# Kernel tuning notes

Hardware: AMD Instinct MI355X
Metric: run time of the kernel (lower is better)

## Reference

```python
import jax, jax.numpy as jnp
import numpy as np

MAX_DISP = 10
KS = 2 * MAX_DISP + 1  # 21 -> 441 displacements


def setup_inputs() -> dict:
    key = jax.random.key(0)
    k1, k2 = jax.random.split(key)
    B, C, H, W = 4, 64, 128, 128
    feat1 = jax.random.normal(k1, (B, C, H, W), dtype=jnp.float32)
    feat2 = jax.random.normal(k2, (B, C, H, W), dtype=jnp.float32)
    return {"feat1": feat1, "feat2": feat2}


def _correlation(feat1, feat2):
    B, C, H, W = feat1.shape
    pad = MAX_DISP
    feat2_p = jnp.pad(feat2, ((0, 0), (0, 0), (pad, pad), (pad, pad)))

    # all (i, j) displacements, flattened row-major to match torch cat order
    ii, jj = jnp.meshgrid(jnp.arange(KS), jnp.arange(KS), indexing="ij")
    shifts = jnp.stack([ii.ravel(), jj.ravel()], axis=-1)  # [KS*KS, 2]

    def one_shift(ij):
        i, j = ij[0], ij[1]
        f2 = jax.lax.dynamic_slice(feat2_p, (0, 0, i, j), (B, C, H, W))
        # reduce over channel dim only; avoid materializing product per-shift
        return jnp.einsum("bchw,bchw->bhw", feat1, f2) / C

    corr = jax.vmap(one_shift)(shifts)            # [KS*KS, B, H, W]
    return jnp.transpose(corr, (1, 0, 2, 3))      # [B, KS*KS, H, W]


def reference(feat1, feat2):
    return _correlation(feat1, feat2)
```

## Files before the change

### kernel.cpp

```cpp
#include <hip/hip_runtime.h>

#define BB  4
#define CC  64
#define HH  128
#define WW  128
#define KS  21
#define PAD 10

__global__ __launch_bounds__(256) void corr_kernel(
    const float* __restrict__ feat1,
    const float* __restrict__ feat2,
    float* __restrict__ out)
{
    const int tid = threadIdx.x;
    int bi = blockIdx.x;
    const int di = bi % KS;  bi /= KS;
    const int h8 = bi % (HH / 8);
    const int b  = bi / (HH / 8);

    const int h  = h8 * 8 + (tid >> 5);
    const int w0 = (tid & 31) << 2;

    const int r = h + di - PAD;

    float acc[4][KS];
#pragma unroll
    for (int p = 0; p < 4; ++p)
#pragma unroll
        for (int d = 0; d < KS; ++d) acc[p][d] = 0.0f;

    if (r >= 0 && r < HH) {
        const float* f1p = feat1 + ((size_t)(b * CC) * HH + h) * WW + w0;
        const float* f2p = feat2 + ((size_t)(b * CC) * HH + r) * WW;

#pragma unroll 2
        for (int c = 0; c < CC; ++c) {
            const float4 a = *(const float4*)(f1p + (size_t)c * (HH * WW));

            float win[28];
#pragma unroll
            for (int j = 0; j < 7; ++j) {
                const int off = w0 - 12 + 4 * j;
                float4 v = make_float4(0.f, 0.f, 0.f, 0.f);
                if (off >= 0 && off < WW)
                    v = *(const float4*)(f2p + (size_t)c * (HH * WW) + off);
                win[4 * j + 0] = v.x;
                win[4 * j + 1] = v.y;
                win[4 * j + 2] = v.z;
                win[4 * j + 3] = v.w;
            }

#pragma unroll
            for (int d = 0; d < KS; ++d) {
                acc[0][d] += a.x * win[d + 2];
                acc[1][d] += a.y * win[d + 3];
                acc[2][d] += a.z * win[d + 4];
                acc[3][d] += a.w * win[d + 5];
            }
        }
    }

    const float scale = 1.0f / (float)CC;
    float* op = out + (((size_t)b * (KS * KS) + (size_t)di * KS) * HH + h) * WW + w0;
#pragma unroll
    for (int d = 0; d < KS; ++d) {
        float4 v = make_float4(acc[0][d] * scale, acc[1][d] * scale,
                               acc[2][d] * scale, acc[3][d] * scale);
        *(float4*)(op + (size_t)d * (HH * WW)) = v;
    }
}

extern "C" void kernel_launch(void* const* d_in, const int* in_sizes, int n_in,
                              void* d_out, int out_size, void* d_ws, size_t ws_size,
                              hipStream_t stream) {
    const float* feat1 = (const float*)d_in[0];
    const float* feat2 = (const float*)d_in[1];
    float* out = (float*)d_out;

    const int blocks = BB * (HH / 8) * KS;
    corr_kernel<<<blocks, 256, 0, stream>>>(feat1, feat2, out);
}
```

Measured before the change: 228.9 us.

## Share feat2 row window through LDS and software-prefetch the next channel

Previously each thread issued seven global float4 loads per channel to build its 28-wide feat2 window. Now each thread loads only its own float4 of feat2 plus small halo pieces. It publishes that float4 into a double-buffered LDS row, and reads neighbour values from the buffer. This relies on each row's threads sitting in one wavefront, so no block barrier is used. Next-channel feat1/feat2 loads are prefetched a step ahead, output uses nontemporal stores, and launch bounds request 3 blocks per CU, trading extra register and LDS pressure for fewer redundant global loads.

```diff
diff --git a/kernel.cpp b/kernel.cpp
--- a/kernel.cpp
+++ b/kernel.cpp
@@ -6,22 +6,37 @@
 #define WW  128
 #define KS  21
 #define PAD 10
+#define HWs (HH*WW)
+#define LROW 160
+#define LBUF (8*LROW)
 
-__global__ __launch_bounds__(256) void corr_kernel(
+typedef float f32x4n __attribute__((ext_vector_type(4)));
+
+__global__ __launch_bounds__(256, 3) void corr_kernel(
     const float* __restrict__ feat1,
     const float* __restrict__ feat2,
     float* __restrict__ out)
 {
+    __shared__ __align__(16) float lds[2*LBUF];
+
     const int tid = threadIdx.x;
     int bi = blockIdx.x;
     const int di = bi % KS;  bi /= KS;
-    const int h8 = bi % (HH / 8);
-    const int b  = bi / (HH / 8);
+    const int h8 = bi % (HH/8);
+    const int b  = bi / (HH/8);
 
-    const int h  = h8 * 8 + (tid >> 5);
-    const int w0 = (tid & 31) << 2;
+    const int row = tid >> 5;
+    const int q   = tid & 31;
+    const int h   = h8*8 + row;
+    const int w0  = q << 2;
+    const int rr  = h + di - PAD;
+    const bool valid = (rr >= 0) && (rr < HH);
 
-    const int r = h + di - PAD;
+    {
+        const int L = (q < 12) ? q : (q + 128);
+        lds[row*LROW + L]        = 0.0f;
+        lds[LBUF + row*LROW + L] = 0.0f;
+    }
 
     float acc[4][KS];
 #pragma unroll
@@ -29,26 +44,61 @@
 #pragma unroll
         for (int d = 0; d < KS; ++d) acc[p][d] = 0.0f;
 
-    if (r >= 0 && r < HH) {
-        const float* f1p = feat1 + ((size_t)(b * CC) * HH + h) * WW + w0;
-        const float* f2p = feat2 + ((size_t)(b * CC) * HH + r) * WW;
+    if (__ballot(valid) != 0ull) {
+        const float* f1p = feat1 + (((ptrdiff_t)b*CC*HH + h)*WW + w0);
+        const float* f2p = feat2 + (((ptrdiff_t)b*CC*HH + rr)*WW + w0);
+
+        float*       lw = &lds[row*LROW + 12 + w0];
+        const float* lr = &lds[row*LROW + w0];
+
+        const bool in0 = valid && (w0 >= 12);
+        const bool in1 = valid && (w0 >= 8);
+
+        float4 vcur = make_float4(0.f,0.f,0.f,0.f);
+        float4 vnxt = make_float4(0.f,0.f,0.f,0.f);
+        float2 g0   = make_float2(0.f,0.f);
+        float4 g1   = make_float4(0.f,0.f,0.f,0.f);
+        if (valid) {
+            vcur = *(const float4*)(f2p);
+            vnxt = *(const float4*)(f2p + HWs);
+        }
+        if (in0) g0 = *(const float2*)(f2p - 10);
+        if (in1) g1 = *(const float4*)(f2p - 8);
+        float4 a = *(const float4*)(f1p);
+
+        *(float4*)lw = vcur;
+        __builtin_amdgcn_sched_barrier(0);
 
 #pragma unroll 2
         for (int c = 0; c < CC; ++c) {
-            const float4 a = *(const float4*)(f1p + (size_t)c * (HH * WW));
+            float4 an  = a;
+            float2 g0n = make_float2(0.f,0.f);
+            float4 g1n = make_float4(0.f,0.f,0.f,0.f);
+            float4 vld = make_float4(0.f,0.f,0.f,0.f);
+            if (c + 1 < CC) {
+                an = *(const float4*)(f1p + HWs);
+                if (in0) g0n = *(const float2*)(f2p + HWs - 10);
+                if (in1) g1n = *(const float4*)(f2p + HWs - 8);
+                if (valid && (c + 2 < CC)) vld = *(const float4*)(f2p + 2*HWs);
+            }
+
+            const float* lrb = lr + ((c & 1) ? LBUF : 0);
+            const float4 w08 = *(const float4*)(lrb + 8);
+            const float4 w16 = *(const float4*)(lrb + 16);
+            const float4 w20 = *(const float4*)(lrb + 20);
+            const float2 w24 = *(const float2*)(lrb + 24);
+
+            *(float4*)(lw + ((c & 1) ? 0 : LBUF)) = vnxt;
+            __builtin_amdgcn_sched_barrier(0);
 
             float win[28];
-#pragma unroll
-            for (int j = 0; j < 7; ++j) {
-                const int off = w0 - 12 + 4 * j;
-                float4 v = make_float4(0.f, 0.f, 0.f, 0.f);
-                if (off >= 0 && off < WW)
-                    v = *(const float4*)(f2p + (size_t)c * (HH * WW) + off);
-                win[4 * j + 0] = v.x;
-                win[4 * j + 1] = v.y;
-                win[4 * j + 2] = v.z;
-                win[4 * j + 3] = v.w;
-            }
+            win[2]=g0.x;   win[3]=g0.y;
+            win[4]=g1.x;   win[5]=g1.y;   win[6]=g1.z;   win[7]=g1.w;
+            win[8]=w08.x;  win[9]=w08.y;  win[10]=w08.z; win[11]=w08.w;
+            win[12]=vcur.x; win[13]=vcur.y; win[14]=vcur.z; win[15]=vcur.w;
+            win[16]=w16.x; win[17]=w16.y; win[18]=w16.z; win[19]=w16.w;
+            win[20]=w20.x; win[21]=w20.y; win[22]=w20.z; win[23]=w20.w;
+            win[24]=w24.x; win[25]=w24.y;
 
 #pragma unroll
             for (int d = 0; d < KS; ++d) {
@@ -57,16 +107,19 @@
                 acc[2][d] += a.z * win[d + 4];
                 acc[3][d] += a.w * win[d + 5];
             }
+
+            a = an; g0 = g0n; g1 = g1n; vcur = vnxt; vnxt = vld;
+            f1p += HWs; f2p += HWs;
         }
     }
 
     const float scale = 1.0f / (float)CC;
-    float* op = out + (((size_t)b * (KS * KS) + (size_t)di * KS) * HH + h) * WW + w0;
+    float* op = out + ((((ptrdiff_t)b*(KS*KS) + di*KS)*HH + h)*WW + w0);
 #pragma unroll
     for (int d = 0; d < KS; ++d) {
-        float4 v = make_float4(acc[0][d] * scale, acc[1][d] * scale,
-                               acc[2][d] * scale, acc[3][d] * scale);
-        *(float4*)(op + (size_t)d * (HH * WW)) = v;
+        f32x4n v = { acc[0][d]*scale, acc[1][d]*scale,
+                     acc[2][d]*scale, acc[3][d]*scale };
+        __builtin_nontemporal_store(v, (f32x4n*)(op + (ptrdiff_t)d*HWs));
     }
 }
 
```

Measured after the change: 211.0 us. 1.08x faster.
